# Kernel optimization log

Hardware: AMD Instinct MI355X
Metric: run time of the kernel (lower is better)

The kernel has to match this reference:

```python
import jax, jax.numpy as jnp
import numpy as np

B, L, D = 64, 1024, 1280

def setup_inputs() -> dict:
    key = jax.random.key(0)
    k1, k2, k3, k4, k5, k6 = jax.random.split(key, 6)
    prev_result = jax.random.normal(k1, (B, L, D), dtype=jnp.float32)
    lengths = jax.random.randint(k2, (B,), 0, 1022)
    dense_w = jax.random.normal(k3, (D, D), dtype=jnp.float32) * 0.02
    dense_b = jax.random.normal(k4, (D,), dtype=jnp.float32) * 0.02
    cls_w = jax.random.normal(k5, (D, 1), dtype=jnp.float32) * 0.02
    cls_b = jax.random.normal(k6, (1,), dtype=jnp.float32) * 0.02
    return {"prev_result": prev_result, "lengths": lengths,
            "dense_w": dense_w, "dense_b": dense_b,
            "cls_w": cls_w, "cls_b": cls_b}

def reference(prev_result, lengths, dense_w, dense_b, cls_w, cls_b):
    # ragged mean pool over first (len + 2) tokens of each sequence
    pool_len = lengths + 2                                  # [B]
    mask = (jnp.arange(L)[None, :] < pool_len[:, None])     # [B, L]
    mask_f = mask.astype(prev_result.dtype)
    summed = jnp.einsum('bld,bl->bd', prev_result, mask_f)  # [B, D]
    embedding = summed / pool_len[:, None].astype(prev_result.dtype)
    x = jax.nn.relu(embedding @ dense_w + dense_b)          # [B, D]
    return x @ cls_w + cls_b                                # [B, 1]
```

## Files before the change

### kernel.cpp

```cpp
#include <hip/hip_runtime.h>

#define BB 64
#define LL 1024
#define DD 1280
#define SPLITS 32
#define CHUNK 32
#define CC 20
#define BG 16

__global__ __launch_bounds__(320) void pool_partial(
    const float* __restrict__ prev, const int* __restrict__ lengths,
    float* __restrict__ P) {
  const int s = blockIdx.x;
  const int b = blockIdx.y;
  const int t = threadIdx.x;

  const int pool_len = lengths[b] + 2;
  const float inv = 1.0f / (float)pool_len;
  const int l0 = s * CHUNK;
  const int l1 = min(pool_len, l0 + CHUNK);

  float4 acc = make_float4(0.f, 0.f, 0.f, 0.f);
  const float* base = prev + (size_t)b * LL * DD + 4 * t;
#pragma unroll 4
  for (int l = l0; l < l1; ++l) {
    const float4 v = *(const float4*)(base + (size_t)l * DD);
    acc.x += v.x; acc.y += v.y; acc.z += v.z; acc.w += v.w;
  }
  acc.x *= inv; acc.y *= inv; acc.z *= inv; acc.w *= inv;
  float4* dst = (float4*)(P + ((size_t)s * BB + b) * DD) + t;
  *dst = acc;
}

__global__ __launch_bounds__(320) void emb_reduce(
    const float* __restrict__ P, const float* __restrict__ cls_b,
    float* __restrict__ emb, float* __restrict__ out) {
  const int b = blockIdx.x;
  const int t = threadIdx.x;

  float4 acc = make_float4(0.f, 0.f, 0.f, 0.f);
#pragma unroll
  for (int s = 0; s < SPLITS; ++s) {
    const float4 v = *((const float4*)(P + ((size_t)s * BB + b) * DD) + t);
    acc.x += v.x; acc.y += v.y; acc.z += v.z; acc.w += v.w;
  }
  *((float4*)(emb + (size_t)b * DD) + t) = acc;
  if (t == 0) out[b] = cls_b[0];
}

__global__ __launch_bounds__(256) void gemm_relu_out(
    const float* __restrict__ emb, const float* __restrict__ W,
    const float* __restrict__ bias, const float* __restrict__ cls_w,
    float* __restrict__ out) {
  __shared__ float es[4 * DD];

  const int cc = blockIdx.x;
  const int bg = blockIdx.y;
  const int t = threadIdx.x;
  const int lane = t & 63;
  const int wave = t >> 6;
  const int b = bg * 4 + wave;
  const int col = cc * 64 + lane;

  const float* eg = emb + (size_t)bg * 4 * DD;
  for (int i = t; i < 4 * DD; i += 256) es[i] = eg[i];
  __syncthreads();

  const float* ew = es + wave * DD;
  const float* wp = W + col;
  float acc = bias[col];
#pragma unroll 32
  for (int d = 0; d < DD; ++d) {
    acc = fmaf(ew[d], wp[(size_t)d * DD], acc);
  }
  float v = fmaxf(acc, 0.f) * cls_w[col];

#pragma unroll
  for (int off = 32; off > 0; off >>= 1) v += __shfl_down(v, off);
  if (lane == 0) atomicAdd(out + b, v);
}

extern "C" void kernel_launch(void* const* d_in, const int* in_sizes, int n_in,
                              void* d_out, int out_size, void* d_ws, size_t ws_size,
                              hipStream_t stream) {
  const float* prev    = (const float*)d_in[0];
  const int*   lengths = (const int*)d_in[1];
  const float* dense_w = (const float*)d_in[2];
  const float* dense_b = (const float*)d_in[3];
  const float* cls_w   = (const float*)d_in[4];
  const float* cls_b   = (const float*)d_in[5];
  float* out = (float*)d_out;

  float* P = (float*)d_ws;
  float* emb = P + (size_t)SPLITS * BB * DD;

  pool_partial<<<dim3(SPLITS, BB), 320, 0, stream>>>(prev, lengths, P);
  emb_reduce<<<BB, 320, 0, stream>>>(P, cls_b, emb, out);
  gemm_relu_out<<<dim3(CC, BG), 256, 0, stream>>>(emb, dense_w, dense_b,
                                                  cls_w, out);
}
```

Baseline: 459.4 us.

## Split GEMM reduction dim across waves, reuse each W load for four batches

```diff
diff --git a/kernel.cpp b/kernel.cpp
--- a/kernel.cpp
+++ b/kernel.cpp
@@ -7,6 +7,7 @@
 #define CHUNK 32
 #define CC 20
 #define BG 16
+#define WD 320
 
 __global__ __launch_bounds__(320) void pool_partial(
     const float* __restrict__ prev, const int* __restrict__ lengths,
@@ -22,7 +23,7 @@
 
   float4 acc = make_float4(0.f, 0.f, 0.f, 0.f);
   const float* base = prev + (size_t)b * LL * DD + 4 * t;
-#pragma unroll 4
+#pragma unroll 8
   for (int l = l0; l < l1; ++l) {
     const float4 v = *(const float4*)(base + (size_t)l * DD);
     acc.x += v.x; acc.y += v.y; acc.z += v.z; acc.w += v.w;
@@ -52,32 +53,51 @@
     const float* __restrict__ emb, const float* __restrict__ W,
     const float* __restrict__ bias, const float* __restrict__ cls_w,
     float* __restrict__ out) {
-  __shared__ float es[4 * DD];
+  __shared__ float4 es4[DD];
+  __shared__ float part[4][4][64];
 
   const int cc = blockIdx.x;
   const int bg = blockIdx.y;
   const int t = threadIdx.x;
   const int lane = t & 63;
   const int wave = t >> 6;
-  const int b = bg * 4 + wave;
   const int col = cc * 64 + lane;
 
   const float* eg = emb + (size_t)bg * 4 * DD;
-  for (int i = t; i < 4 * DD; i += 256) es[i] = eg[i];
+  float* est = (float*)es4;
+#pragma unroll
+  for (int k = 0; k < 20; ++k) {
+    const int i = k * 256 + t;
+    const int j = i / DD;
+    const int d = i - j * DD;
+    est[d * 4 + j] = eg[i];
+  }
   __syncthreads();
 
-  const float* ew = es + wave * DD;
-  const float* wp = W + col;
-  float acc = bias[col];
-#pragma unroll 32
-  for (int d = 0; d < DD; ++d) {
-    acc = fmaf(ew[d], wp[(size_t)d * DD], acc);
+  const float* wp = W + (size_t)wave * WD * DD + col;
+  float a0 = 0.f, a1 = 0.f, a2 = 0.f, a3 = 0.f;
+#pragma unroll 8
+  for (int d = 0; d < WD; ++d) {
+    const float wv = wp[(size_t)d * DD];
+    const float4 e = es4[wave * WD + d];
+    a0 = fmaf(e.x, wv, a0);
+    a1 = fmaf(e.y, wv, a1);
+    a2 = fmaf(e.z, wv, a2);
+    a3 = fmaf(e.w, wv, a3);
   }
-  float v = fmaxf(acc, 0.f) * cls_w[col];
+  part[wave][0][lane] = a0;
+  part[wave][1][lane] = a1;
+  part[wave][2][lane] = a2;
+  part[wave][3][lane] = a3;
+  __syncthreads();
+
+  float v = part[0][wave][lane] + part[1][wave][lane] +
+            part[2][wave][lane] + part[3][wave][lane] + bias[col];
+  v = fmaxf(v, 0.f) * cls_w[col];
 
 #pragma unroll
   for (int off = 32; off > 0; off >>= 1) v += __shfl_down(v, off);
-  if (lane == 0) atomicAdd(out + b, v);
+  if (lane == 0) atomicAdd(out + bg * 4 + wave, v);
 }
 
 extern "C" void kernel_launch(void* const* d_in, const int* in_sizes, int n_in,
```

Result: faster. 447.7 us (-2.5%).
